# Optimization experiments

Measured on AMD Instinct MI355X. Metric: run time of the kernel, lower is better.

## Reference

```python
import jax, jax.numpy as jnp
import numpy as np

COMMITMENT_FACTOR = 0.25
QUANTIZATION_FACTOR = 1.0


def setup_inputs() -> dict:
    key = jax.random.key(0)
    k1, k2 = jax.random.split(key)
    B, D, H, W = 64, 256, 32, 32
    K = 1024
    z = jax.random.normal(k1, (B, D, H, W), dtype=jnp.float32)
    # torch init: uniform(-1/K, 1/K)
    codebook = jax.random.uniform(k2, (K, D), dtype=jnp.float32,
                                  minval=-1.0 / K, maxval=1.0 / K)
    return {"z": z, "codebook": codebook}


def reference(z, codebook):
    # z: [B, D, H, W]; codebook: [K, D]
    B, D, H, W = z.shape
    z_nhwc = jnp.transpose(z, (0, 2, 3, 1))          # [B, H, W, D]
    z_flat = z_nhwc.reshape(-1, D)                    # [N, D]
    # squared euclidean distances: ||z||^2 + ||w||^2 - 2 z.w
    dist = (jnp.sum(z_flat ** 2, axis=-1, keepdims=True)
            + jnp.sum(codebook ** 2, axis=-1)
            - 2.0 * z_flat @ codebook.T)              # [N, K]
    closest = jnp.argmin(dist, axis=-1)               # [N]
    quantized_indices = closest.reshape(B, H, W)
    # one-hot @ codebook == gather
    q_flat = codebook[closest]                        # [N, D]
    quantized = q_flat.reshape(B, H, W, D)

    commitment_loss = jnp.sum((jax.lax.stop_gradient(quantized) - z_nhwc) ** 2)
    embedding_loss = jnp.sum((quantized - jax.lax.stop_gradient(z_nhwc)) ** 2)
    loss = commitment_loss * COMMITMENT_FACTOR + embedding_loss * QUANTIZATION_FACTOR

    # straight-through estimator
    quantized_st = z_nhwc + jax.lax.stop_gradient(quantized - z_nhwc)
    quantized_st = jnp.transpose(quantized_st, (0, 3, 1, 2))  # [B, D, H, W]
    quantized_indices = quantized_indices[:, None, :, :]       # [B, 1, H, W]
    return quantized_st, quantized_indices, loss
```

## Files before the change

kernel.cpp:

```cpp
#include <hip/hip_runtime.h>


#define IDX_OFF  16777216
#define LOSS_OFF 16842752

typedef __bf16 bf16x8 __attribute__((ext_vector_type(8)));
typedef float  f32x4  __attribute__((ext_vector_type(4)));

__global__ __launch_bounds__(256) void vq_prep(const float* __restrict__ cb,
                                               __bf16* __restrict__ cbh,
                                               float* __restrict__ sc1) {
    const int t = threadIdx.x;
    const int r = blockIdx.x * 16 + (t >> 4);
    const int d0 = (t & 15) * 16;
    const float* src = cb + (size_t)r * 256 + d0;
    __bf16* dst = cbh + (size_t)r * 256 + d0;
    float s = 0.f;
    float4 f[4];
    #pragma unroll
    for (int p = 0; p < 4; p++) f[p] = *(const float4*)(src + p * 4);
    bf16x8 v0, v1;
    #pragma unroll
    for (int p = 0; p < 4; p++) {
        s = fmaf(f[p].x, f[p].x, s); s = fmaf(f[p].y, f[p].y, s);
        s = fmaf(f[p].z, f[p].z, s); s = fmaf(f[p].w, f[p].w, s);
    }
    v0[0]=(__bf16)f[0].x; v0[1]=(__bf16)f[0].y; v0[2]=(__bf16)f[0].z; v0[3]=(__bf16)f[0].w;
    v0[4]=(__bf16)f[1].x; v0[5]=(__bf16)f[1].y; v0[6]=(__bf16)f[1].z; v0[7]=(__bf16)f[1].w;
    v1[0]=(__bf16)f[2].x; v1[1]=(__bf16)f[2].y; v1[2]=(__bf16)f[2].z; v1[3]=(__bf16)f[2].w;
    v1[4]=(__bf16)f[3].x; v1[5]=(__bf16)f[3].y; v1[6]=(__bf16)f[3].z; v1[7]=(__bf16)f[3].w;
    *(bf16x8*)dst = v0;
    *(bf16x8*)(dst + 8) = v1;
    s += __shfl_xor(s, 1, 64);
    s += __shfl_xor(s, 2, 64);
    s += __shfl_xor(s, 4, 64);
    s += __shfl_xor(s, 8, 64);
    if ((t & 15) == 0) sc1[r] = s + 1.0f;
}

__global__ __launch_bounds__(256, 2) void vq_mfma(const float* __restrict__ z,
                                                  const __bf16* __restrict__ cbh,
                                                  const float* __restrict__ sc1,
                                                  float* __restrict__ out) {
    __shared__ __align__(16) __bf16 z_s[128 * 256];
    __shared__ float red_s[4];

    const int t    = threadIdx.x;
    const int lane = t & 63;
    const int w    = t >> 6;
    const int m16  = lane & 15;
    const int q4   = lane >> 4;
    const int wn   = (w >> 1) * 64;
    const int wk   = (w & 1) * 64;
    const int blk  = blockIdx.x;
    const int b    = blk >> 3;
    const int hw0  = (blk & 7) << 7;
    const int n0   = blk << 7;

    bf16x8 bb[4];
    {
        const __bf16* bp = cbh + (size_t)(wk + m16) * 256 + q4 * 8;
        #pragma unroll
        for (int j = 0; j < 4; j++) bb[j] = *(const bf16x8*)(bp + (size_t)j * 4096);
    }

    float lz = 0.f;
    {
        const int nl    = t & 127;
        const int dhalf = (t >> 7) << 7;
        const float* zp = z + (size_t)(b * 256 + dhalf) * 1024 + hw0 + nl;
        #pragma unroll
        for (int p = 0; p < 16; p++) {
            bf16x8 v;
            #pragma unroll
            for (int j = 0; j < 8; j++) {
                float f = zp[(size_t)(p * 8 + j) * 1024];
                lz = fmaf(f, f, lz);
                v[j] = (__bf16)f;
            }
            int gs = ((dhalf >> 3) + p) ^ (nl & 7);
            *(bf16x8*)&z_s[nl * 256 + gs * 8] = v;
        }
    }
    __syncthreads();

    unsigned int best[16];
    #pragma unroll
    for (int i = 0; i < 16; i++) best[i] = 0xFFFFFFFFu;

    const int arow = wn + m16;
    #pragma unroll 1
    for (int kt = 0; kt < 1024; kt += 128) {
        int   kcv[4];
        float sck[4];
        #pragma unroll
        for (int j = 0; j < 4; j++) {
            kcv[j] = kt + wk + j * 16 + m16;
            sck[j] = sc1[kcv[j]];
        }
        const __bf16* bc  = cbh + (size_t)(kt + wk + m16) * 256 + q4 * 8;
        const int ktn = (kt + 128) & 1023;
        const __bf16* bnx = cbh + (size_t)(ktn + wk + m16) * 256 + q4 * 8;

        f32x4 acc[4][4];
        #pragma unroll
        for (int i = 0; i < 4; i++)
            #pragma unroll
            for (int j = 0; j < 4; j++) acc[i][j] = (f32x4){0.f, 0.f, 0.f, 0.f};

        #pragma unroll
        for (int dc = 0; dc < 256; dc += 32) {
            bf16x8 bn[4];
            const __bf16* bp = (dc == 224) ? bnx : (bc + dc + 32);
            #pragma unroll
            for (int j = 0; j < 4; j++) bn[j] = *(const bf16x8*)(bp + (size_t)j * 4096);

            bf16x8 a[4];
            const int gs = ((dc >> 3) + q4) ^ (m16 & 7);
            #pragma unroll
            for (int i = 0; i < 4; i++)
                a[i] = *(const bf16x8*)&z_s[(arow + i * 16) * 256 + gs * 8];

            #pragma unroll
            for (int i = 0; i < 4; i++)
                #pragma unroll
                for (int j = 0; j < 4; j++)
                    acc[i][j] = __builtin_amdgcn_mfma_f32_16x16x32_bf16(a[i], bb[j], acc[i][j], 0, 0, 0);

            #pragma unroll
            for (int j = 0; j < 4; j++) bb[j] = bn[j];
        }

        #pragma unroll
        for (int j = 0; j < 4; j++) {
            #pragma unroll
            for (int i = 0; i < 4; i++)
                #pragma unroll
                for (int r = 0; r < 4; r++) {
                    float v3 = fmaf(-2.f, acc[i][j][r], sck[j]);
                    unsigned int key = (__float_as_uint(v3) & 0xFFFFFC00u) | (unsigned int)kcv[j];
                    int pos = i * 4 + r;
                    best[pos] = min(best[pos], key);
                }
        }
    }

    #pragma unroll
    for (int pos = 0; pos < 16; pos++) {
        unsigned int k = best[pos];
        #pragma unroll
        for (int off = 1; off < 16; off <<= 1)
            k = min(k, (unsigned int)__shfl_xor((int)k, off, 64));
        best[pos] = k;
    }
    __syncthreads();

    unsigned int* ks = (unsigned int*)z_s;
    if (m16 == 0) {
        #pragma unroll
        for (int pos = 0; pos < 16; pos++) {
            int i = pos >> 2, r = pos & 3;
            int row = wn + i * 16 + q4 * 4 + r;
            ks[(w & 1) * 128 + row] = best[pos];
        }
    }
    __syncthreads();
    if (t < 128) {
        unsigned int key = min(ks[t], ks[128 + t]);
        int kf = (int)(key & 1023u);
        ks[512 + t] = (unsigned int)kf;
        out[IDX_OFF + n0 + t] = (float)kf;
        lz += __uint_as_float(key & 0xFFFFFC00u) - 1.0f;
    }
    {
        float s = lz;
        #pragma unroll
        for (int off = 1; off < 64; off <<= 1) s += __shfl_xor(s, off, 64);
        if (lane == 0) red_s[w] = s;
    }
    __syncthreads();
    if (t == 0)
        atomicAdd(out + LOSS_OFF, 1.25f * ((red_s[0] + red_s[1]) + (red_s[2] + red_s[3])));

    const int qrow = t >> 1;
    const int qoff = (t & 1) * 128;
    const int myk  = (int)ks[512 + qrow];
    __syncthreads();
    {
        const __bf16* qp = cbh + (size_t)myk * 256 + qoff;
        #pragma unroll
        for (int p = 0; p < 16; p++) {
            bf16x8 v = *(const bf16x8*)(qp + p * 8);
            int gs = ((qoff >> 3) + p) ^ (qrow & 7);
            *(bf16x8*)&z_s[qrow * 256 + gs * 8] = v;
        }
    }
    __syncthreads();
    {
        const int nl    = t & 127;
        const int dhalf = (t >> 7) << 7;
        float* op = out + (size_t)(b * 256 + dhalf) * 1024 + hw0 + nl;
        #pragma unroll
        for (int p = 0; p < 16; p++) {
            int gs = ((dhalf >> 3) + p) ^ (nl & 7);
            bf16x8 v = *(const bf16x8*)&z_s[nl * 256 + gs * 8];
            #pragma unroll
            for (int j = 0; j < 8; j++)
                op[(size_t)(p * 8 + j) * 1024] = (float)v[j];
        }
    }
}

extern "C" void kernel_launch(void* const* d_in, const int* in_sizes, int n_in,
                              void* d_out, int out_size, void* d_ws, size_t ws_size,
                              hipStream_t stream) {
    const float* z  = (const float*)d_in[0];
    const float* cb = (const float*)d_in[1];
    float* out = (float*)d_out;

    float*  sc1 = (float*)d_ws;
    __bf16* cbh = (__bf16*)((char*)d_ws + 8192);

    hipMemsetAsync(out + LOSS_OFF, 0, sizeof(float), stream);
    vq_prep<<<64, 256, 0, stream>>>(cb, cbh, sc1);
    vq_mfma<<<512, 256, 0, stream>>>(z, cbh, sc1, out);
}
```

Baseline: 192.8 us.

## Halve row tile, relayout bf16 codebook into d-chunks, fold -2 scale into z

Each block now handles 64 spatial positions instead of 128, which halves shared memory and raises the occupancy target to 4 blocks per CU. The grid doubles to 1024 blocks. The bf16 codebook is stored in 32-wide d-chunk-major layout so each B-fragment load is contiguous, and z is pre-scaled by -2 so the accumulators can start at the codebook norms and the per-element fmaf is dropped. The A fragments are prefetched from LDS one step ahead. The final gather reads the fp32 codebook and rounds it to bf16. The loss zeroing moves into the prep kernel, replacing the memset. The trade-off is that each block re-streams the whole codebook against half as many rows, so total codebook traffic doubles.

```diff
diff --git a/kernel.cpp b/kernel.cpp
--- a/kernel.cpp
+++ b/kernel.cpp
@@ -9,26 +9,28 @@
 
 __global__ __launch_bounds__(256) void vq_prep(const float* __restrict__ cb,
                                                __bf16* __restrict__ cbh,
-                                               float* __restrict__ sc1) {
+                                               float* __restrict__ sc1,
+                                               float* __restrict__ out) {
+    if (blockIdx.x == 0 && threadIdx.x == 0) out[LOSS_OFF] = 0.f;
     const int t = threadIdx.x;
     const int r = blockIdx.x * 16 + (t >> 4);
     const int d0 = (t & 15) * 16;
     const float* src = cb + (size_t)r * 256 + d0;
-    __bf16* dst = cbh + (size_t)r * 256 + d0;
     float s = 0.f;
     float4 f[4];
     #pragma unroll
     for (int p = 0; p < 4; p++) f[p] = *(const float4*)(src + p * 4);
-    bf16x8 v0, v1;
     #pragma unroll
     for (int p = 0; p < 4; p++) {
         s = fmaf(f[p].x, f[p].x, s); s = fmaf(f[p].y, f[p].y, s);
         s = fmaf(f[p].z, f[p].z, s); s = fmaf(f[p].w, f[p].w, s);
     }
+    bf16x8 v0, v1;
     v0[0]=(__bf16)f[0].x; v0[1]=(__bf16)f[0].y; v0[2]=(__bf16)f[0].z; v0[3]=(__bf16)f[0].w;
     v0[4]=(__bf16)f[1].x; v0[5]=(__bf16)f[1].y; v0[6]=(__bf16)f[1].z; v0[7]=(__bf16)f[1].w;
     v1[0]=(__bf16)f[2].x; v1[1]=(__bf16)f[2].y; v1[2]=(__bf16)f[2].z; v1[3]=(__bf16)f[2].w;
     v1[4]=(__bf16)f[3].x; v1[5]=(__bf16)f[3].y; v1[6]=(__bf16)f[3].z; v1[7]=(__bf16)f[3].w;
+    __bf16* dst = cbh + (size_t)(d0 >> 5) * 32768 + r * 32 + (d0 & 31);
     *(bf16x8*)dst = v0;
     *(bf16x8*)(dst + 8) = v1;
     s += __shfl_xor(s, 1, 64);
@@ -38,11 +40,12 @@
     if ((t & 15) == 0) sc1[r] = s + 1.0f;
 }
 
-__global__ __launch_bounds__(256, 2) void vq_mfma(const float* __restrict__ z,
+__global__ __launch_bounds__(256, 4) void vq_mfma(const float* __restrict__ z,
+                                                  const float* __restrict__ cb,
                                                   const __bf16* __restrict__ cbh,
                                                   const float* __restrict__ sc1,
                                                   float* __restrict__ out) {
-    __shared__ __align__(16) __bf16 z_s[128 * 256];
+    __shared__ __align__(16) __bf16 z_s[64 * 256];
     __shared__ float red_s[4];
 
     const int t    = threadIdx.x;
@@ -50,103 +53,111 @@
     const int w    = t >> 6;
     const int m16  = lane & 15;
     const int q4   = lane >> 4;
-    const int wn   = (w >> 1) * 64;
+    const int wn   = (w >> 1) * 32;
     const int wk   = (w & 1) * 64;
     const int blk  = blockIdx.x;
-    const int b    = blk >> 3;
-    const int hw0  = (blk & 7) << 7;
-    const int n0   = blk << 7;
-
+    const int b    = blk >> 4;
+    const int hw0  = (blk & 15) << 6;
+    const int n0   = blk << 6;
+
+    const __bf16* bbase = cbh + (size_t)(wk + m16) * 32 + q4 * 8;
+
+    float sck[4];
+    #pragma unroll
+    for (int j = 0; j < 4; j++) sck[j] = sc1[wk + j * 16 + m16];
     bf16x8 bb[4];
-    {
-        const __bf16* bp = cbh + (size_t)(wk + m16) * 256 + q4 * 8;
-        #pragma unroll
-        for (int j = 0; j < 4; j++) bb[j] = *(const bf16x8*)(bp + (size_t)j * 4096);
-    }
+    #pragma unroll
+    for (int j = 0; j < 4; j++) bb[j] = *(const bf16x8*)(bbase + j * 512);
 
     float lz = 0.f;
     {
-        const int nl    = t & 127;
-        const int dhalf = (t >> 7) << 7;
-        const float* zp = z + (size_t)(b * 256 + dhalf) * 1024 + hw0 + nl;
-        #pragma unroll
-        for (int p = 0; p < 16; p++) {
+        const int nl = t & 63;
+        const int dq = (t >> 6) << 6;
+        const float* zp = z + (size_t)(b * 256 + dq) * 1024 + hw0 + nl;
+        #pragma unroll
+        for (int p = 0; p < 8; p++) {
             bf16x8 v;
             #pragma unroll
             for (int j = 0; j < 8; j++) {
                 float f = zp[(size_t)(p * 8 + j) * 1024];
                 lz = fmaf(f, f, lz);
-                v[j] = (__bf16)f;
+                v[j] = (__bf16)(-2.0f * f);
             }
-            int gs = ((dhalf >> 3) + p) ^ (nl & 7);
+            int gs = ((dq >> 3) + p) ^ (nl & 7);
             *(bf16x8*)&z_s[nl * 256 + gs * 8] = v;
         }
     }
     __syncthreads();
 
-    unsigned int best[16];
-    #pragma unroll
-    for (int i = 0; i < 16; i++) best[i] = 0xFFFFFFFFu;
-
-    const int arow = wn + m16;
+    bf16x8 a[2];
+    #pragma unroll
+    for (int i = 0; i < 2; i++) {
+        int gs = q4 ^ (m16 & 7);
+        a[i] = *(const bf16x8*)&z_s[(wn + i * 16 + m16) * 256 + gs * 8];
+    }
+
+    unsigned int best[8];
+    #pragma unroll
+    for (int i = 0; i < 8; i++) best[i] = 0xFFFFFFFFu;
+
     #pragma unroll 1
-    for (int kt = 0; kt < 1024; kt += 128) {
-        int   kcv[4];
-        float sck[4];
+    for (int kts = 0; kts < 8; kts++) {
+        float sckn[4];
+        const int knext = (((kts + 1) & 7) << 7) + wk;
+        #pragma unroll
+        for (int j = 0; j < 4; j++) sckn[j] = sc1[knext + j * 16 + m16];
+
+        f32x4 acc[2][4];
         #pragma unroll
         for (int j = 0; j < 4; j++) {
-            kcv[j] = kt + wk + j * 16 + m16;
-            sck[j] = sc1[kcv[j]];
-        }
-        const __bf16* bc  = cbh + (size_t)(kt + wk + m16) * 256 + q4 * 8;
-        const int ktn = (kt + 128) & 1023;
-        const __bf16* bnx = cbh + (size_t)(ktn + wk + m16) * 256 + q4 * 8;
-
-        f32x4 acc[4][4];
-        #pragma unroll
-        for (int i = 0; i < 4; i++)
-            #pragma unroll
-            for (int j = 0; j < 4; j++) acc[i][j] = (f32x4){0.f, 0.f, 0.f, 0.f};
-
-        #pragma unroll
-        for (int dc = 0; dc < 256; dc += 32) {
-            bf16x8 bn[4];
-            const __bf16* bp = (dc == 224) ? bnx : (bc + dc + 32);
-            #pragma unroll
-            for (int j = 0; j < 4; j++) bn[j] = *(const bf16x8*)(bp + (size_t)j * 4096);
-
-            bf16x8 a[4];
-            const int gs = ((dc >> 3) + q4) ^ (m16 & 7);
-            #pragma unroll
-            for (int i = 0; i < 4; i++)
-                a[i] = *(const bf16x8*)&z_s[(arow + i * 16) * 256 + gs * 8];
-
-            #pragma unroll
-            for (int i = 0; i < 4; i++)
+            f32x4 iv = (f32x4){sck[j], sck[j], sck[j], sck[j]};
+            acc[0][j] = iv; acc[1][j] = iv;
+        }
+
+        const __bf16* bk  = bbase + (size_t)(kts << 7) * 32;
+        const __bf16* bkn = bbase + (size_t)(((kts + 1) & 7) << 7) * 32;
+
+        #pragma unroll
+        for (int c = 0; c < 8; c++) {
+            bf16x8 bn[4], an[2];
+            const __bf16* bp = (c == 7) ? bkn : (bk + (size_t)(c + 1) * 32768);
+            #pragma unroll
+            for (int j = 0; j < 4; j++) bn[j] = *(const bf16x8*)(bp + j * 512);
+            const int cn = (c + 1) & 7;
+            #pragma unroll
+            for (int i = 0; i < 2; i++) {
+                int gs = (cn * 4 + q4) ^ (m16 & 7);
+                an[i] = *(const bf16x8*)&z_s[(wn + i * 16 + m16) * 256 + gs * 8];
+            }
+
+            #pragma unroll
+            for (int i = 0; i < 2; i++)
                 #pragma unroll
                 for (int j = 0; j < 4; j++)
                     acc[i][j] = __builtin_amdgcn_mfma_f32_16x16x32_bf16(a[i], bb[j], acc[i][j], 0, 0, 0);
 
             #pragma unroll
             for (int j = 0; j < 4; j++) bb[j] = bn[j];
+            a[0] = an[0]; a[1] = an[1];
         }
 
         #pragma unroll
         for (int j = 0; j < 4; j++) {
-            #pragma unroll
-            for (int i = 0; i < 4; i++)
+            const unsigned int kc = (unsigned int)((kts << 7) + wk + j * 16 + m16);
+            #pragma unroll
+            for (int i = 0; i < 2; i++)
                 #pragma unroll
                 for (int r = 0; r < 4; r++) {
-                    float v3 = fmaf(-2.f, acc[i][j][r], sck[j]);
-                    unsigned int key = (__float_as_uint(v3) & 0xFFFFFC00u) | (unsigned int)kcv[j];
-                    int pos = i * 4 + r;
-                    best[pos] = min(best[pos], key);
+                    unsigned int key = (__float_as_uint(acc[i][j][r]) & 0xFFFFFC00u) | kc;
+                    best[i * 4 + r] = min(best[i * 4 + r], key);
                 }
         }
-    }
-
-    #pragma unroll
-    for (int pos = 0; pos < 16; pos++) {
+        #pragma unroll
+        for (int j = 0; j < 4; j++) sck[j] = sckn[j];
+    }
+
+    #pragma unroll
+    for (int pos = 0; pos < 8; pos++) {
         unsigned int k = best[pos];
         #pragma unroll
         for (int off = 1; off < 16; off <<= 1)
@@ -158,17 +169,17 @@
     unsigned int* ks = (unsigned int*)z_s;
     if (m16 == 0) {
         #pragma unroll
-        for (int pos = 0; pos < 16; pos++) {
+        for (int pos = 0; pos < 8; pos++) {
             int i = pos >> 2, r = pos & 3;
             int row = wn + i * 16 + q4 * 4 + r;
-            ks[(w & 1) * 128 + row] = best[pos];
-        }
-    }
-    __syncthreads();
-    if (t < 128) {
-        unsigned int key = min(ks[t], ks[128 + t]);
+            ks[(w & 1) * 64 + row] = best[pos];
+        }
+    }
+    __syncthreads();
+    if (t < 64) {
+        unsigned int key = min(ks[t], ks[64 + t]);
         int kf = (int)(key & 1023u);
-        ks[512 + t] = (unsigned int)kf;
+        ks[128 + t] = (unsigned int)kf;
         out[IDX_OFF + n0 + t] = (float)kf;
         lz += __uint_as_float(key & 0xFFFFFC00u) - 1.0f;
     }
@@ -182,27 +193,31 @@
     if (t == 0)
         atomicAdd(out + LOSS_OFF, 1.25f * ((red_s[0] + red_s[1]) + (red_s[2] + red_s[3])));
 
-    const int qrow = t >> 1;
-    const int qoff = (t & 1) * 128;
-    const int myk  = (int)ks[512 + qrow];
-    __syncthreads();
-    {
-        const __bf16* qp = cbh + (size_t)myk * 256 + qoff;
-        #pragma unroll
-        for (int p = 0; p < 16; p++) {
-            bf16x8 v = *(const bf16x8*)(qp + p * 8);
+    const int qrow = t >> 2;
+    const int qoff = (t & 3) * 64;
+    const int myk  = (int)ks[128 + qrow];
+    __syncthreads();
+    {
+        const float* qp = cb + (size_t)myk * 256 + qoff;
+        #pragma unroll
+        for (int p = 0; p < 8; p++) {
+            float4 f0 = *(const float4*)(qp + p * 8);
+            float4 f1 = *(const float4*)(qp + p * 8 + 4);
+            bf16x8 v;
+            v[0]=(__bf16)f0.x; v[1]=(__bf16)f0.y; v[2]=(__bf16)f0.z; v[3]=(__bf16)f0.w;
+            v[4]=(__bf16)f1.x; v[5]=(__bf16)f1.y; v[6]=(__bf16)f1.z; v[7]=(__bf16)f1.w;
             int gs = ((qoff >> 3) + p) ^ (qrow & 7);
             *(bf16x8*)&z_s[qrow * 256 + gs * 8] = v;
         }
     }
     __syncthreads();
     {
-        const int nl    = t & 127;
-        const int dhalf = (t >> 7) << 7;
-        float* op = out + (size_t)(b * 256 + dhalf) * 1024 + hw0 + nl;
-        #pragma unroll
-        for (int p = 0; p < 16; p++) {
-            int gs = ((dhalf >> 3) + p) ^ (nl & 7);
+        const int nl = t & 63;
+        const int dq = (t >> 6) << 6;
+        float* op = out + (size_t)(b * 256 + dq) * 1024 + hw0 + nl;
+        #pragma unroll
+        for (int p = 0; p < 8; p++) {
+            int gs = ((dq >> 3) + p) ^ (nl & 7);
             bf16x8 v = *(const bf16x8*)&z_s[nl * 256 + gs * 8];
             #pragma unroll
             for (int j = 0; j < 8; j++)
@@ -221,7 +236,6 @@
     float*  sc1 = (float*)d_ws;
     __bf16* cbh = (__bf16*)((char*)d_ws + 8192);
 
-    hipMemsetAsync(out + LOSS_OFF, 0, sizeof(float), stream);
-    vq_prep<<<64, 256, 0, stream>>>(cb, cbh, sc1);
-    vq_mfma<<<512, 256, 0, stream>>>(z, cbh, sc1, out);
+    vq_prep<<<64, 256, 0, stream>>>(cb, cbh, sc1, out);
+    vq_mfma<<<1024, 256, 0, stream>>>(z, cb, cbh, sc1, out);
 }
```

New measurement: 200.3 us. 1.04x slower.
